# Kernel tuning notes

Measured on AMD Instinct MI355X. Metric: run time of the kernel, lower is better.

## Reference

```python
import jax, jax.numpy as jnp
import numpy as np

TAU_MEM = 20.0
V_THRESH = 1.0
DECAY = float(np.exp(-1.0 / TAU_MEM))
SLOPE = 5.0  # fast-sigmoid surrogate slope


@jax.custom_vjp
def spike(x):
    # Heaviside spike with fast-sigmoid surrogate gradient
    return (x > 0).astype(x.dtype)

def _spike_fwd(x):
    return spike(x), x

def _spike_bwd(x, g):
    surr = 1.0 / (1.0 + SLOPE * jnp.abs(x)) ** 2
    return (g * surr,)

spike.defvjp(_spike_fwd, _spike_bwd)


def setup_inputs() -> dict:
    key = jax.random.key(0)
    k1, k2 = jax.random.split(key)
    B, T, n_in, n_out = 32, 1000, 1024, 512
    input_spikes_seq = (jax.random.uniform(k1, (B, T, n_in)) < 0.05).astype(jnp.float32)
    w_init_scale = 0.5
    W = jax.random.normal(k2, (n_out, n_in), dtype=jnp.float32) * (w_init_scale / np.sqrt(n_in))
    return {"input_spikes_seq": input_spikes_seq, "W": W}


def reference(input_spikes_seq, W):
    # input_spikes_seq: (B, T, n_in); W: (n_out, n_in) -> out: (B, T, n_out)
    B, T, _ = input_spikes_seq.shape
    n_out = W.shape[0]
    # Hoist the GEMM out of the time loop: (B,T,n_in) x (n_out,n_in) -> (B,T,n_out)
    I = jnp.einsum('bti,oi->bto', input_spikes_seq, W)
    I_t = jnp.transpose(I, (1, 0, 2))  # (T, B, n_out)

    def step(v, i_t):
        v = v * DECAY + i_t
        s = spike(v - V_THRESH)
        v = v * (1.0 - jax.lax.stop_gradient(s))  # reset, detached as in torch
        return v, s

    v0 = jnp.zeros((B, n_out), dtype=input_spikes_seq.dtype)
    _, out_t = jax.lax.scan(step, v0, I_t)  # out_t: (T, B, n_out)
    return jnp.transpose(out_t, (1, 0, 2))
```

## Files before the change

### kernel.cpp

```cpp
#include <hip/hip_runtime.h>


#define N_IN   1024
#define N_OUT  512
#define DECAY_F 0.95122942450071400910f
#define SCALE     17179869184.0
#define SCALE_INV 5.8207660913467407e-11f

typedef int  v4i  __attribute__((ext_vector_type(4)));
typedef int  v16i __attribute__((ext_vector_type(16)));

__global__ __launch_bounds__(256) void s_to_i8(const float* __restrict__ S,
                                               signed char* __restrict__ S8,
                                               int n16) {
    const int g = blockIdx.x * 256 + threadIdx.x;
    if (g >= n16) return;
    const float4* p = reinterpret_cast<const float4*>(S) + (size_t)g * 4;
    union { signed char c[16]; int4 v; } u;
#pragma unroll
    for (int q = 0; q < 4; ++q) {
        const float4 v = p[q];
        u.c[q * 4 + 0] = (signed char)(v.x != 0.f);
        u.c[q * 4 + 1] = (signed char)(v.y != 0.f);
        u.c[q * 4 + 2] = (signed char)(v.z != 0.f);
        u.c[q * 4 + 3] = (signed char)(v.w != 0.f);
    }
    reinterpret_cast<int4*>(S8)[g] = u.v;
}

__global__ __launch_bounds__(256) void w_digits(const float* __restrict__ W,
                                                signed char* __restrict__ D8) {
    const int n  = blockIdx.x;
    const int k0 = threadIdx.x * 4;
    const float4 wv = *reinterpret_cast<const float4*>(W + (size_t)n * N_IN + k0);
    const float ww[4] = {wv.x, wv.y, wv.z, wv.w};
    int pk[4] = {0, 0, 0, 0};
#pragma unroll
    for (int j = 0; j < 4; ++j) {
        long long wi = (long long)rint((double)ww[j] * SCALE);
        const int d0 = (int)((wi + 128) & 255) - 128; wi = (wi - d0) >> 8;
        const int d1 = (int)((wi + 128) & 255) - 128; wi = (wi - d1) >> 8;
        const int d2 = (int)((wi + 128) & 255) - 128; wi = (wi - d2) >> 8;
        const int d3 = (int)wi;
        pk[0] |= (d0 & 255) << (8 * j);
        pk[1] |= (d1 & 255) << (8 * j);
        pk[2] |= (d2 & 255) << (8 * j);
        pk[3] |= (d3 & 255) << (8 * j);
    }
#pragma unroll
    for (int d = 0; d < 4; ++d)
        *reinterpret_cast<int*>(D8 + (size_t)(d * N_OUT + n) * N_IN + k0) = pk[d];
}

#define BM 256
#define BN 64
#define BK 64
#define PITCH 80
#define ABUF (BM * PITCH)
#define ASH(buf) (lds + (buf) * ABUF)
#define BSH(buf) (lds + 2 * ABUF + (buf) * ABUF)

__global__ __launch_bounds__(512, 2) void gemm_i8(
        const signed char* __restrict__ S8,
        const signed char* __restrict__ D8,
        float* __restrict__ I, int M) {
    extern __shared__ signed char lds[];

    const int tid  = threadIdx.x;
    const int lane = tid & 63;
    const int w    = tid >> 6;
    const int wwm  = w >> 1;
    const int wwn  = w & 1;
    const int bn = blockIdx.x & 7;
    const int bm = blockIdx.x >> 3;
    const int m0 = bm * BM;
    const int n0 = bn * BN;

    const int srow = tid >> 2;
    const int scol = (tid & 3) * 16;

    v16i acc[2][4];
#pragma unroll
    for (int mf = 0; mf < 2; ++mf)
#pragma unroll
        for (int d = 0; d < 4; ++d)
#pragma unroll
            for (int i = 0; i < 16; ++i) acc[mf][d][i] = 0;

    int4 ra0, ra1, rb0, rb1;
#define LOADT(kt)                                                                 \
    ra0 = *reinterpret_cast<const int4*>(S8 + (size_t)(m0 + srow) * N_IN + (kt) * BK + scol);        \
    ra1 = *reinterpret_cast<const int4*>(S8 + (size_t)(m0 + srow + 128) * N_IN + (kt) * BK + scol);  \
    rb0 = *reinterpret_cast<const int4*>(D8 + (size_t)(((srow >> 6) * N_OUT) + n0 + (srow & 63)) * N_IN + (kt) * BK + scol);            \
    rb1 = *reinterpret_cast<const int4*>(D8 + (size_t)(((srow >> 6) * N_OUT + 2 * N_OUT) + n0 + (srow & 63)) * N_IN + (kt) * BK + scol);

#define WRITET(buf)                                                               \
    *reinterpret_cast<int4*>(ASH(buf) + (srow) * PITCH + scol) = ra0;             \
    *reinterpret_cast<int4*>(ASH(buf) + (srow + 128) * PITCH + scol) = ra1;       \
    *reinterpret_cast<int4*>(BSH(buf) + (srow) * PITCH + scol) = rb0;             \
    *reinterpret_cast<int4*>(BSH(buf) + (srow + 128) * PITCH + scol) = rb1;

    LOADT(0);
    WRITET(0);
    __syncthreads();

    const int fr = lane & 31;
    const int kh = (lane >> 5) * 16;

    int cur = 0;
#pragma unroll 1
    for (int kt = 0; kt < N_IN / BK; ++kt) {
        if (kt < N_IN / BK - 1) { LOADT(kt + 1); }
#pragma unroll
        for (int ksub = 0; ksub < 2; ++ksub) {
            const int kb = ksub * 32 + kh;
            v4i af0 = *reinterpret_cast<const v4i*>(
                ASH(cur) + (wwm * 64 + fr) * PITCH + kb);
            v4i af1 = *reinterpret_cast<const v4i*>(
                ASH(cur) + (wwm * 64 + 32 + fr) * PITCH + kb);
            v4i bf[4];
#pragma unroll
            for (int d = 0; d < 4; ++d)
                bf[d] = *reinterpret_cast<const v4i*>(
                    BSH(cur) + (d * 64 + wwn * 32 + fr) * PITCH + kb);
#pragma unroll
            for (int d = 0; d < 4; ++d) {
                acc[0][d] = __builtin_amdgcn_mfma_i32_32x32x32_i8(af0, bf[d], acc[0][d], 0, 0, 0);
                acc[1][d] = __builtin_amdgcn_mfma_i32_32x32x32_i8(af1, bf[d], acc[1][d], 0, 0, 0);
            }
        }
        if (kt < N_IN / BK - 1) { WRITET(cur ^ 1); }
        __syncthreads();
        cur ^= 1;
    }

    const int col = fr;
    const int rb_ = (lane >> 5) * 4;
#pragma unroll
    for (int mf = 0; mf < 2; ++mf) {
#pragma unroll
        for (int reg = 0; reg < 16; ++reg) {
            const int row = (reg & 3) + 8 * (reg >> 2) + rb_;
            const long long v =
                ((long long)acc[mf][3][reg] << 24) + ((long long)acc[mf][2][reg] << 16) +
                ((long long)acc[mf][1][reg] << 8) + (long long)acc[mf][0][reg];
            I[(size_t)(m0 + wwm * 64 + mf * 32 + row) * N_OUT + n0 + wwn * 32 + col] =
                (float)v * SCALE_INV;
        }
    }
}
#undef LOADT
#undef WRITET

#define UNROLL_T 40
__global__ __launch_bounds__(256) void lif_scan2(float* __restrict__ IO, int T) {
    const int idx = blockIdx.x * blockDim.x + threadIdx.x;
    const int b = idx >> 9, o = idx & (N_OUT - 1);
    float* p = IO + (size_t)b * T * N_OUT + o;
    float v = 0.f;
    for (int t0 = 0; t0 < T; t0 += UNROLL_T) {
        float c[UNROLL_T];
#pragma unroll
        for (int j = 0; j < UNROLL_T; ++j) c[j] = p[(size_t)(t0 + j) * N_OUT];
#pragma unroll
        for (int j = 0; j < UNROLL_T; ++j) {
            v = v * DECAY_F + c[j];
            float s = (v > 1.0f) ? 1.0f : 0.f;
            v *= (1.f - s);
            c[j] = s;
        }
#pragma unroll
        for (int j = 0; j < UNROLL_T; ++j) p[(size_t)(t0 + j) * N_OUT] = c[j];
    }
}

__global__ __launch_bounds__(256) void transpose_w(const float* __restrict__ W,
                                                   float* __restrict__ WT) {
    __shared__ float t[32][33];
    const int k0 = blockIdx.x * 32;
    const int n0 = blockIdx.y * 32;
    const int lx = threadIdx.x & 31;
    const int ly = threadIdx.x >> 5;
#pragma unroll
    for (int r = ly; r < 32; r += 8)
        t[r][lx] = W[(size_t)(n0 + r) * N_IN + k0 + lx];
    __syncthreads();
#pragma unroll
    for (int r = ly; r < 32; r += 8)
        WT[(size_t)(k0 + r) * N_OUT + n0 + lx] = t[lx][r];
}

__global__ __launch_bounds__(256) void gather_rows(
        const float* __restrict__ S, const float* __restrict__ WT,
        float* __restrict__ I, int M) {
    const int wid  = blockIdx.x * 4 + (threadIdx.x >> 6);
    const int lane = threadIdx.x & 63;
    if (wid >= M) return;
    const float* srow = S + (size_t)wid * N_IN;
    float4 a0 = {0.f, 0.f, 0.f, 0.f};
    float4 a1 = {0.f, 0.f, 0.f, 0.f};
    float sv[16];
#pragma unroll
    for (int g = 0; g < 16; ++g) sv[g] = srow[g * 64 + lane];
#pragma unroll
    for (int g = 0; g < 16; ++g) {
        unsigned long long m = __ballot(sv[g] != 0.0f);
        while (m) {
            const int b = __builtin_ctzll(m);
            m &= m - 1;
            const int k = g * 64 + b;
            const float* wp = WT + (size_t)k * N_OUT + lane * 4;
            const float4 w0 = *reinterpret_cast<const float4*>(wp);
            const float4 w1 = *reinterpret_cast<const float4*>(wp + 256);
            a0.x += w0.x; a0.y += w0.y; a0.z += w0.z; a0.w += w0.w;
            a1.x += w1.x; a1.y += w1.y; a1.z += w1.z; a1.w += w1.w;
        }
    }
    float* op = I + (size_t)wid * N_OUT + lane * 4;
    *reinterpret_cast<float4*>(op) = a0;
    *reinterpret_cast<float4*>(op + 256) = a1;
}

extern "C" void kernel_launch(void* const* d_in, const int* in_sizes, int n_in,
                              void* d_out, int out_size, void* d_ws, size_t ws_size,
                              hipStream_t stream) {
    const float* S = (const float*)d_in[0];
    const float* W = (const float*)d_in[1];
    float* out = (float*)d_out;

    const int K = N_IN;
    const int M = in_sizes[0] / K;
    const int B = 32;
    const int T = M / B;

    const size_t s8_bytes = (size_t)M * N_IN;
    const size_t d8_bytes = (size_t)4 * N_OUT * N_IN;
    const size_t need = s8_bytes + d8_bytes;

    if (ws_size >= need && (M % BM) == 0) {
        signed char* S8 = (signed char*)d_ws;
        signed char* D8 = (signed char*)d_ws + s8_bytes;
        const int n16 = M * N_IN / 16;
        s_to_i8<<<(n16 + 255) / 256, 256, 0, stream>>>(S, S8, n16);
        w_digits<<<N_OUT, 256, 0, stream>>>(W, D8);
        const size_t lds_bytes = (size_t)4 * ABUF;
        gemm_i8<<<(M / BM) * (N_OUT / BN), 512, lds_bytes, stream>>>(S8, D8, out, M);
        lif_scan2<<<(B * N_OUT) / 256, 256, 0, stream>>>(out, T);
    } else if (ws_size >= (size_t)N_IN * N_OUT * sizeof(float) && (M % 4) == 0) {
        float* WT = (float*)d_ws;
        dim3 tg(N_IN / 32, N_OUT / 32);
        transpose_w<<<tg, 256, 0, stream>>>(W, WT);
        gather_rows<<<M / 4, 256, 0, stream>>>(S, WT, out, M);
        lif_scan2<<<(B * N_OUT) / 256, 256, 0, stream>>>(out, T);
    }
}
```

Measured before the change: 147.5 us.

## Deepen int8 GEMM prefetch to two tiles, swizzle block order, raise MFMA priority

The int8 GEMM main loop is restructured to keep two K-tiles in flight in registers (p/q sets) while computing from alternating LDS buffers, unrolled by two. This aims to hide global load latency better than the single-tile prefetch did. Block indices are remapped so consecutive workgroups cover different tiles, which is meant to improve L2 reuse of the spike and weight tiles. s_setprio is raised around the MFMA bursts. In exchange, register pressure rises under the 512-thread, 2-block launch bound, which risks spills or lower occupancy.

```diff
diff --git a/kernel.cpp b/kernel.cpp
--- a/kernel.cpp
+++ b/kernel.cpp
@@ -71,8 +71,11 @@
     const int w    = tid >> 6;
     const int wwm  = w >> 1;
     const int wwn  = w & 1;
-    const int bn = blockIdx.x & 7;
-    const int bm = blockIdx.x >> 3;
+
+    const int nx  = M / BM;
+    const int u   = (blockIdx.x & 7) * nx + (blockIdx.x >> 3);
+    const int bm  = u >> 3;
+    const int bn  = u & 7;
     const int m0 = bm * BM;
     const int n0 = bn * BN;
 
@@ -87,51 +90,61 @@
 #pragma unroll
             for (int i = 0; i < 16; ++i) acc[mf][d][i] = 0;
 
-    int4 ra0, ra1, rb0, rb1;
-#define LOADT(kt)                                                                 \
-    ra0 = *reinterpret_cast<const int4*>(S8 + (size_t)(m0 + srow) * N_IN + (kt) * BK + scol);        \
-    ra1 = *reinterpret_cast<const int4*>(S8 + (size_t)(m0 + srow + 128) * N_IN + (kt) * BK + scol);  \
-    rb0 = *reinterpret_cast<const int4*>(D8 + (size_t)(((srow >> 6) * N_OUT) + n0 + (srow & 63)) * N_IN + (kt) * BK + scol);            \
-    rb1 = *reinterpret_cast<const int4*>(D8 + (size_t)(((srow >> 6) * N_OUT + 2 * N_OUT) + n0 + (srow & 63)) * N_IN + (kt) * BK + scol);
-
-#define WRITET(buf)                                                               \
-    *reinterpret_cast<int4*>(ASH(buf) + (srow) * PITCH + scol) = ra0;             \
-    *reinterpret_cast<int4*>(ASH(buf) + (srow + 128) * PITCH + scol) = ra1;       \
-    *reinterpret_cast<int4*>(BSH(buf) + (srow) * PITCH + scol) = rb0;             \
-    *reinterpret_cast<int4*>(BSH(buf) + (srow + 128) * PITCH + scol) = rb1;
-
-    LOADT(0);
-    WRITET(0);
-    __syncthreads();
+    int4 pa0, pa1, pb0, pb1;
+    int4 qa0, qa1, qb0, qb1;
+
+#define LOADT(SET, kt)                                                            \
+    SET##a0 = *reinterpret_cast<const int4*>(S8 + (size_t)(m0 + srow) * N_IN + (kt) * BK + scol);        \
+    SET##a1 = *reinterpret_cast<const int4*>(S8 + (size_t)(m0 + srow + 128) * N_IN + (kt) * BK + scol);  \
+    SET##b0 = *reinterpret_cast<const int4*>(D8 + (size_t)(((srow >> 6) * N_OUT) + n0 + (srow & 63)) * N_IN + (kt) * BK + scol);            \
+    SET##b1 = *reinterpret_cast<const int4*>(D8 + (size_t)(((srow >> 6) * N_OUT + 2 * N_OUT) + n0 + (srow & 63)) * N_IN + (kt) * BK + scol);
+
+#define WRITET(buf, SET)                                                          \
+    *reinterpret_cast<int4*>(ASH(buf) + (srow) * PITCH + scol) = SET##a0;         \
+    *reinterpret_cast<int4*>(ASH(buf) + (srow + 128) * PITCH + scol) = SET##a1;   \
+    *reinterpret_cast<int4*>(BSH(buf) + (srow) * PITCH + scol) = SET##b0;         \
+    *reinterpret_cast<int4*>(BSH(buf) + (srow + 128) * PITCH + scol) = SET##b1;
 
     const int fr = lane & 31;
     const int kh = (lane >> 5) * 16;
 
-    int cur = 0;
+#define COMPUTE(buf)                                                              \
+    _Pragma("unroll")                                                             \
+    for (int ksub = 0; ksub < 2; ++ksub) {                                        \
+        const int kb = ksub * 32 + kh;                                            \
+        v4i af0 = *reinterpret_cast<const v4i*>(ASH(buf) + (wwm * 64 + fr) * PITCH + kb);       \
+        v4i af1 = *reinterpret_cast<const v4i*>(ASH(buf) + (wwm * 64 + 32 + fr) * PITCH + kb);  \
+        v4i bf[4];                                                                \
+        _Pragma("unroll")                                                         \
+        for (int d = 0; d < 4; ++d)                                               \
+            bf[d] = *reinterpret_cast<const v4i*>(BSH(buf) + (d * 64 + wwn * 32 + fr) * PITCH + kb); \
+        __builtin_amdgcn_s_setprio(1);                                            \
+        _Pragma("unroll")                                                         \
+        for (int d = 0; d < 4; ++d) {                                             \
+            acc[0][d] = __builtin_amdgcn_mfma_i32_32x32x32_i8(af0, bf[d], acc[0][d], 0, 0, 0); \
+            acc[1][d] = __builtin_amdgcn_mfma_i32_32x32x32_i8(af1, bf[d], acc[1][d], 0, 0, 0); \
+        }                                                                         \
+        __builtin_amdgcn_s_setprio(0);                                            \
+    }
+
+    LOADT(p, 0);
+    WRITET(0, p);
+    LOADT(p, 1);
+    LOADT(q, 2);
+    __syncthreads();
+
 #pragma unroll 1
-    for (int kt = 0; kt < N_IN / BK; ++kt) {
-        if (kt < N_IN / BK - 1) { LOADT(kt + 1); }
-#pragma unroll
-        for (int ksub = 0; ksub < 2; ++ksub) {
-            const int kb = ksub * 32 + kh;
-            v4i af0 = *reinterpret_cast<const v4i*>(
-                ASH(cur) + (wwm * 64 + fr) * PITCH + kb);
-            v4i af1 = *reinterpret_cast<const v4i*>(
-                ASH(cur) + (wwm * 64 + 32 + fr) * PITCH + kb);
-            v4i bf[4];
-#pragma unroll
-            for (int d = 0; d < 4; ++d)
-                bf[d] = *reinterpret_cast<const v4i*>(
-                    BSH(cur) + (d * 64 + wwn * 32 + fr) * PITCH + kb);
-#pragma unroll
-            for (int d = 0; d < 4; ++d) {
-                acc[0][d] = __builtin_amdgcn_mfma_i32_32x32x32_i8(af0, bf[d], acc[0][d], 0, 0, 0);
-                acc[1][d] = __builtin_amdgcn_mfma_i32_32x32x32_i8(af1, bf[d], acc[1][d], 0, 0, 0);
-            }
-        }
-        if (kt < N_IN / BK - 1) { WRITET(cur ^ 1); }
+    for (int kt = 0; kt < 16; kt += 2) {
+        WRITET(1, p);
+        if (kt + 3 <= 15) { LOADT(p, kt + 3); }
+        COMPUTE(0);
         __syncthreads();
-        cur ^= 1;
+        if (kt + 2 <= 15) {
+            WRITET(0, q);
+            if (kt + 4 <= 15) { LOADT(q, kt + 4); }
+        }
+        COMPUTE(1);
+        __syncthreads();
     }
 
     const int col = fr;
@@ -151,6 +164,7 @@
 }
 #undef LOADT
 #undef WRITET
+#undef COMPUTE
 
 #define UNROLL_T 40
 __global__ __launch_bounds__(256) void lif_scan2(float* __restrict__ IO, int T) {
```

After: 142.1 us. 3.6% less time.
